# Kernel tuning notes

Measured on AMD Instinct MI355X. Metric: run time of the kernel, lower is better.

## Reference

```python
import jax, jax.numpy as jnp
import numpy as np

N_NODES = 100000
N_EDGES = 1600000
F_IN = 48
F_HID = 64


def setup_inputs() -> dict:
    key = jax.random.key(0)
    k1, k2, k3, k4 = jax.random.split(key, 4)
    x = jax.random.normal(k1, (N_NODES, F_IN), dtype=jnp.float32)
    edge_index = jax.random.randint(k2, (2, N_EDGES), 0, N_NODES, dtype=jnp.int64)
    W1 = jax.random.normal(k3, (F_IN, F_HID), dtype=jnp.float32) * (1.0 / np.sqrt(F_IN))
    b1 = jnp.zeros((F_HID,), dtype=jnp.float32)
    W2 = jax.random.normal(k4, (F_HID, 2), dtype=jnp.float32) * (1.0 / np.sqrt(F_HID))
    b2 = jnp.zeros((2,), dtype=jnp.float32)
    return {"x": x, "edge_index": edge_index, "W1": W1, "b1": b1, "W2": W2, "b2": b2}


def _gcn_prep(edge_index, n_nodes):
    # PyG GCNConv default: add self-loops, symmetric normalization D^-1/2 (A+I) D^-1/2
    loops = jnp.arange(n_nodes, dtype=edge_index.dtype)
    src = jnp.concatenate([edge_index[0], loops])
    dst = jnp.concatenate([edge_index[1], loops])
    deg = jax.ops.segment_sum(jnp.ones_like(dst, dtype=jnp.float32), dst,
                              num_segments=n_nodes)
    dinv = jnp.where(deg > 0, jax.lax.rsqrt(deg), 0.0)
    norm = dinv[src] * dinv[dst]  # [E+N]
    return src, dst, norm


def _gcn_conv(h, W, b, src, dst, norm, n_nodes):
    h = h @ W                          # [N, F_out] linear first (PyG order)
    msg = h[src] * norm[:, None]       # gather + edge-scale
    agg = jax.ops.segment_sum(msg, dst, num_segments=n_nodes)  # scatter-add
    return agg + b


def reference(x, edge_index, W1, b1, W2, b2):
    n = x.shape[0]
    src, dst, norm = _gcn_prep(edge_index, n)
    h = jax.nn.relu(_gcn_conv(x, W1, b1, src, dst, norm, n))
    return _gcn_conv(h, W2, b2, src, dst, norm, n)
```

## Files before the change

kernel.cpp:

```cpp
#include <hip/hip_runtime.h>
#include <hip/hip_fp16.h>

#define F_IN 48
#define F_HID 64
#define GSH 7
#define GSZ 128
#define MAXB 1024
#define CAPSH 12
#define CAP 4096
#define CHUNK 4096
#define NPW 16

__device__ __forceinline__ bool detect64(const int* __restrict__ e) {
    return ((e[1] | e[3] | e[5] | e[7]) == 0);
}
__device__ __forceinline__ int load_src(const int* e, int i, int E, bool is64) {
    return e[is64 ? (long)2 * i : (long)i];
}
__device__ __forceinline__ int load_dst(const int* e, int i, int E, bool is64) {
    return e[is64 ? (long)2 * (E + i) : (long)(E + i)];
}
__device__ __forceinline__ void fmix2(float& alo, float& ahi, unsigned h) {
    asm("v_fma_mix_f32 %0, %2, 1.0, %0 op_sel_hi:[1,0,0]\n\t"
        "v_fma_mix_f32 %1, %2, 1.0, %1 op_sel:[1,0,0] op_sel_hi:[1,0,0]"
        : "+v"(alo), "+v"(ahi) : "v"(h));
}

__global__ __launch_bounds__(256) void passA(const int* __restrict__ e,
                                             int* __restrict__ bcnt,
                                             int* __restrict__ ebuf, int E, int B) {
    __shared__ int lcnt[MAXB], lbase[MAXB];
    bool is64 = detect64(e);
    bool vec = ((E & 3) == 0);
    int base = blockIdx.x * CHUNK;
    for (int t = threadIdx.x; t < B; t += 256) lcnt[t] = 0;
    __syncthreads();
    int pk[16], bk[16], rk[16];
#pragma unroll
    for (int g = 0; g < 4; ++g) {
        int i = base + (((g << 8) + (int)threadIdx.x) << 2);
        int r = g * 4;
        if (vec && i + 3 < E) {
            int4 s4, d4;
            if (is64) {
                const int4* p = (const int4*)(e + (size_t)2 * i);
                int4 a = p[0], bb = p[1];
                s4 = make_int4(a.x, a.z, bb.x, bb.z);
                const int4* q = (const int4*)(e + (size_t)2 * E + (size_t)2 * i);
                int4 c = q[0], dd = q[1];
                d4 = make_int4(c.x, c.z, dd.x, dd.z);
            } else {
                s4 = *(const int4*)(e + i);
                d4 = *(const int4*)(e + E + i);
            }
            int ss[4] = {s4.x, s4.y, s4.z, s4.w};
            int dv[4] = {d4.x, d4.y, d4.z, d4.w};
#pragma unroll
            for (int u = 0; u < 4; ++u) {
                pk[r + u] = ss[u] | ((dv[u] & (GSZ - 1)) << 17);
                bk[r + u] = dv[u] >> GSH;
                rk[r + u] = atomicAdd(&lcnt[bk[r + u]], 1);
            }
        } else {
#pragma unroll
            for (int u = 0; u < 4; ++u) {
                int ii = i + u;
                if (ii < E) {
                    int s = load_src(e, ii, E, is64);
                    int d = load_dst(e, ii, E, is64);
                    pk[r + u] = s | ((d & (GSZ - 1)) << 17);
                    bk[r + u] = d >> GSH;
                    rk[r + u] = atomicAdd(&lcnt[bk[r + u]], 1);
                } else {
                    bk[r + u] = -1;
                }
            }
        }
    }
    __syncthreads();
    for (int t = threadIdx.x; t < B; t += 256) {
        int c = lcnt[t];
        lbase[t] = c ? atomicAdd(&bcnt[t], c) : 0;
    }
    __syncthreads();
#pragma unroll
    for (int r = 0; r < 16; ++r) {
        if (bk[r] >= 0) {
            int pos = lbase[bk[r]] + rk[r];
            if (pos < CAP) ebuf[((size_t)bk[r] << CAPSH) + pos] = pk[r];
        }
    }
}

__global__ __launch_bounds__(256) void passB(const int* __restrict__ ebuf,
                                             const int* __restrict__ bcnt,
                                             int* __restrict__ rowStart,
                                             int* __restrict__ deg,
                                             float* __restrict__ dinv,
                                             int* __restrict__ srcSorted, int N) {
    __shared__ int cnt[GSZ], inc[GSZ], exo[GSZ];
    int b = blockIdx.x, t = threadIdx.x;
    int m = min(bcnt[b], CAP);
    const int* eb = ebuf + ((size_t)b << CAPSH);
    if (t < GSZ) cnt[t] = 0;
    __syncthreads();
    int gk[16], sk[16], rk[16];
    int iters = (m + 255) >> 8;
    for (int it = 0; it < iters; ++it) {
        int i = t + (it << 8);
        if (i < m) {
            int pkv = eb[i];
            gk[it] = pkv >> 17;
            sk[it] = pkv & 0x1FFFF;
            rk[it] = atomicAdd(&cnt[gk[it]], 1);
        } else {
            gk[it] = -1;
        }
    }
    __syncthreads();
    int myc = (t < GSZ) ? cnt[t] : 0;
    if (t < GSZ) inc[t] = myc;
    __syncthreads();
    for (int o = 1; o < GSZ; o <<= 1) {
        int v = (t < GSZ && t >= o) ? inc[t - o] : 0;
        __syncthreads();
        if (t < GSZ) inc[t] += v;
        __syncthreads();
    }
    if (t < GSZ) {
        int ex = inc[t] - myc;
        exo[t] = ex;
        int node = (b << GSH) + t;
        if (node < N) {
            rowStart[node] = (b << CAPSH) + ex;
            deg[node] = myc;
            dinv[node] = rsqrtf((float)myc + 1.0f);
        }
    }
    __syncthreads();
    int s0b = b << CAPSH;
    for (int it = 0; it < iters; ++it) {
        if (gk[it] >= 0)
            srcSorted[s0b + exo[gk[it]] + rk[it]] = sk[it];
    }
}

__global__ __launch_bounds__(256) void gemm1(const float* __restrict__ x,
                                             const float* __restrict__ W1,
                                             const float* __restrict__ dinv,
                                             __half* __restrict__ H, int N) {
    const int lane = threadIdx.x & 63;
    const int warp = __builtin_amdgcn_readfirstlane((int)(threadIdx.x >> 6));
    const int nb = (blockIdx.x * 4 + warp) * NPW;
    float w[F_IN];
#pragma unroll
    for (int k = 0; k < F_IN; ++k) w[k] = W1[k * F_HID + lane];
    for (int u = 0; u < NPW; u += 2) {
        int na = nb + u, nb2 = nb + u + 1;
        int nac = min(na, N - 1), nbc = min(nb2, N - 1);
        const float* xra = x + (size_t)nac * F_IN;
        const float* xrb = x + (size_t)nbc * F_IN;
        float ha = 0.0f, hb = 0.0f;
#pragma unroll
        for (int k = 0; k < F_IN; ++k) {
            ha = fmaf(xra[k], w[k], ha);
            hb = fmaf(xrb[k], w[k], hb);
        }
        if (na < N)
            H[(size_t)na * F_HID + lane] = __float2half(dinv[nac] * ha);
        if (nb2 < N)
            H[(size_t)nb2 * F_HID + lane] = __float2half(dinv[nbc] * hb);
    }
}

__global__ __launch_bounds__(256) void agg1(const __half* __restrict__ H,
                                            const float* __restrict__ b1,
                                            const float* __restrict__ W2,
                                            const float* __restrict__ dinv,
                                            const int* __restrict__ rowStart,
                                            const int* __restrict__ deg,
                                            const int* __restrict__ srcSorted,
                                            float* __restrict__ g2, int N) {
    const int lane = threadIdx.x & 63;
    const int sub = lane >> 5;
    const int fl = lane & 31;
    const int base = blockIdx.x * 16 + (threadIdx.x >> 6) * 4;
    const char* hb = (const char*)H;
    const unsigned fb = (unsigned)fl << 2;

    int n0 = base, n1 = base + 1, n2 = base + 2, n3 = base + 3;
    int dn0 = (n0 < N) ? deg[n0] : -1;
    int dn1 = (n1 < N) ? deg[n1] : -1;
    int dn2_ = (n2 < N) ? deg[n2] : -1;
    int dn3 = (n3 < N) ? deg[n3] : -1;
    int rs0 = (n0 < N) ? rowStart[n0] : 0;
    int rs1 = (n1 < N) ? rowStart[n1] : 0;
    int rs2 = (n2 < N) ? rowStart[n2] : 0;
    int rs3 = (n3 < N) ? rowStart[n3] : 0;

    int idx0 = N, idx1 = N, idx2 = N, idx3 = N;
    if (lane < dn0) idx0 = srcSorted[rs0 + lane]; else if (lane == dn0) idx0 = n0;
    if (lane < dn1) idx1 = srcSorted[rs1 + lane]; else if (lane == dn1) idx1 = n1;
    if (lane < dn2_) idx2 = srcSorted[rs2 + lane]; else if (lane == dn2_) idx2 = n2;
    if (lane < dn3) idx3 = srcSorted[rs3 + lane]; else if (lane == dn3) idx3 = n3;

    float ax0 = 0, ay0 = 0, ax1 = 0, ay1 = 0;
    float ax2 = 0, ay2 = 0, ax3 = 0, ay3 = 0;

    auto batch6 = [&](int p0) {
        unsigned o[6][4], v[6][4];
#pragma unroll
        for (int p = 0; p < 6; ++p) {
            int sA = 2 * (p0 + p) + sub;
            o[p][0] = ((unsigned)__shfl(idx0, sA, 64) << 7) + fb;
            o[p][1] = ((unsigned)__shfl(idx1, sA, 64) << 7) + fb;
            o[p][2] = ((unsigned)__shfl(idx2, sA, 64) << 7) + fb;
            o[p][3] = ((unsigned)__shfl(idx3, sA, 64) << 7) + fb;
        }
#pragma unroll
        for (int p = 0; p < 6; ++p) {
            v[p][0] = *(const unsigned*)(hb + o[p][0]);
            v[p][1] = *(const unsigned*)(hb + o[p][1]);
            v[p][2] = *(const unsigned*)(hb + o[p][2]);
            v[p][3] = *(const unsigned*)(hb + o[p][3]);
        }
#pragma unroll
        for (int p = 0; p < 6; ++p) {
            fmix2(ax0, ay0, v[p][0]);
            fmix2(ax1, ay1, v[p][1]);
            fmix2(ax2, ay2, v[p][2]);
            fmix2(ax3, ay3, v[p][3]);
        }
    };
    batch6(0);
    batch6(6);

    int maxD = max(max(dn0, dn1), max(dn2_, dn3));
    int maxSlot = maxD + 1;
    for (int p = 12; p < 32 && 2 * p < maxSlot; ++p) {
        int sA = 2 * p + sub;
        unsigned o0 = ((unsigned)__shfl(idx0, sA, 64) << 7) + fb;
        unsigned o1 = ((unsigned)__shfl(idx1, sA, 64) << 7) + fb;
        unsigned o2 = ((unsigned)__shfl(idx2, sA, 64) << 7) + fb;
        unsigned o3 = ((unsigned)__shfl(idx3, sA, 64) << 7) + fb;
        unsigned v0 = *(const unsigned*)(hb + o0);
        unsigned v1 = *(const unsigned*)(hb + o1);
        unsigned v2 = *(const unsigned*)(hb + o2);
        unsigned v3 = *(const unsigned*)(hb + o3);
        fmix2(ax0, ay0, v0);
        fmix2(ax1, ay1, v1);
        fmix2(ax2, ay2, v2);
        fmix2(ax3, ay3, v3);
    }
    if (maxSlot > 64) {
        const __half2* hp = (const __half2*)H;
        for (int s = 64; s < maxSlot; ++s) {
            if (sub == 0) {
                if (s <= dn0) { float2 f = __half22float2(hp[((long)((s < dn0) ? srcSorted[rs0 + s] : n0) << 5) + fl]); ax0 += f.x; ay0 += f.y; }
                if (s <= dn1) { float2 f = __half22float2(hp[((long)((s < dn1) ? srcSorted[rs1 + s] : n1) << 5) + fl]); ax1 += f.x; ay1 += f.y; }
                if (s <= dn2_) { float2 f = __half22float2(hp[((long)((s < dn2_) ? srcSorted[rs2 + s] : n2) << 5) + fl]); ax2 += f.x; ay2 += f.y; }
                if (s <= dn3) { float2 f = __half22float2(hp[((long)((s < dn3) ? srcSorted[rs3 + s] : n3) << 5) + fl]); ax3 += f.x; ay3 += f.y; }
            }
        }
    }

    ax0 += __shfl(ax0, lane ^ 32, 64); ay0 += __shfl(ay0, lane ^ 32, 64);
    ax1 += __shfl(ax1, lane ^ 32, 64); ay1 += __shfl(ay1, lane ^ 32, 64);
    ax2 += __shfl(ax2, lane ^ 32, 64); ay2 += __shfl(ay2, lane ^ 32, 64);
    ax3 += __shfl(ax3, lane ^ 32, 64); ay3 += __shfl(ay3, lane ^ 32, 64);
    float di0 = (n0 < N) ? dinv[n0] : 0.0f;
    float di1 = (n1 < N) ? dinv[n1] : 0.0f;
    float di2 = (n2 < N) ? dinv[n2] : 0.0f;
    float di3 = (n3 < N) ? dinv[n3] : 0.0f;

    float2 b1v = *(const float2*)(b1 + 2 * fl);
    float4 w2q = *(const float4*)(W2 + 4 * fl);
    float hA, hB;
    hA = fmaxf(fmaf(di0, ax0, b1v.x), 0.0f); hB = fmaxf(fmaf(di0, ay0, b1v.y), 0.0f);
    float t00 = hA * w2q.x + hB * w2q.z, t01 = hA * w2q.y + hB * w2q.w;
    hA = fmaxf(fmaf(di1, ax1, b1v.x), 0.0f); hB = fmaxf(fmaf(di1, ay1, b1v.y), 0.0f);
    float t10 = hA * w2q.x + hB * w2q.z, t11 = hA * w2q.y + hB * w2q.w;
    hA = fmaxf(fmaf(di2, ax2, b1v.x), 0.0f); hB = fmaxf(fmaf(di2, ay2, b1v.y), 0.0f);
    float t20 = hA * w2q.x + hB * w2q.z, t21 = hA * w2q.y + hB * w2q.w;
    hA = fmaxf(fmaf(di3, ax3, b1v.x), 0.0f); hB = fmaxf(fmaf(di3, ay3, b1v.y), 0.0f);
    float t30 = hA * w2q.x + hB * w2q.z, t31 = hA * w2q.y + hB * w2q.w;
#pragma unroll
    for (int m = 1; m <= 16; m <<= 1) {
        t00 += __shfl_xor(t00, m, 64); t01 += __shfl_xor(t01, m, 64);
        t10 += __shfl_xor(t10, m, 64); t11 += __shfl_xor(t11, m, 64);
        t20 += __shfl_xor(t20, m, 64); t21 += __shfl_xor(t21, m, 64);
        t30 += __shfl_xor(t30, m, 64); t31 += __shfl_xor(t31, m, 64);
    }
    if (lane == 0) {
        float2* g2v = (float2*)g2;
        if (n0 < N) g2v[n0] = make_float2(di0 * t00, di0 * t01);
        if (n1 < N) g2v[n1] = make_float2(di1 * t10, di1 * t11);
        if (n2 < N) g2v[n2] = make_float2(di2 * t20, di2 * t21);
        if (n3 < N) g2v[n3] = make_float2(di3 * t30, di3 * t31);
    }
}

__global__ __launch_bounds__(256) void agg2(const int* __restrict__ rowStart,
                                            const int* __restrict__ deg,
                                            const int* __restrict__ srcSorted,
                                            const float* __restrict__ g2,
                                            const float* __restrict__ dinv,
                                            const float* __restrict__ b2,
                                            float* __restrict__ out, int N) {
    int gid = blockIdx.x * 256 + threadIdx.x;
    int node = gid >> 4, l16 = gid & 15;
    if (node >= N) return;
    const char* gb = (const char*)g2;
    int rs = rowStart[node], dn = deg[node];
    float a0 = 0.0f, a1 = 0.0f;
    for (int j = l16; j < dn; j += 16) {
        unsigned o = (unsigned)srcSorted[rs + j] << 3;
        float2 v = *(const float2*)(gb + o);
        a0 += v.x;
        a1 += v.y;
    }
#pragma unroll
    for (int m = 1; m < 16; m <<= 1) {
        a0 += __shfl_xor(a0, m, 64);
        a1 += __shfl_xor(a1, m, 64);
    }
    if (l16 == 0) {
        float2 self = *(const float2*)(gb + ((unsigned)node << 3));
        float di = dinv[node];
        out[2 * node + 0] = di * (a0 + self.x) + b2[0];
        out[2 * node + 1] = di * (a1 + self.y) + b2[1];
    }
}

extern "C" void kernel_launch(void* const* d_in, const int* in_sizes, int n_in,
                              void* d_out, int out_size, void* d_ws, size_t ws_size,
                              hipStream_t stream) {
    const float* x  = (const float*)d_in[0];
    const int* eidx = (const int*)d_in[1];
    const float* W1 = (const float*)d_in[2];
    const float* b1 = (const float*)d_in[3];
    const float* W2 = (const float*)d_in[4];
    const float* b2 = (const float*)d_in[5];
    float* out = (float*)d_out;

    int N = in_sizes[0] / F_IN;
    int E = in_sizes[1] / 2;
    int B = (N + GSZ - 1) >> GSH;

    char* ws = (char*)d_ws;
    __half* H         = (__half*)ws;   ws += (size_t)(N + 1) * F_HID * 2;
    int*    bcnt      = (int*)ws;      ws += MAXB * 4;
    int*    deg       = (int*)ws;      ws += (size_t)N * 4;
    int*    rowStart  = (int*)ws;      ws += (size_t)N * 4;
    float*  dinv      = (float*)ws;    ws += (size_t)N * 4;
    float*  g2        = (float*)ws;    ws += (size_t)N * 2 * 4;
    ws = (char*)(((size_t)ws + 255) & ~(size_t)255);
    int*    ebuf      = (int*)ws;      ws += (size_t)MAXB * CAP * 4;
    int*    srcSorted = (int*)ws;      ws += (size_t)MAXB * CAP * 4;

    hipMemsetAsync(H + (size_t)N * F_HID, 0, 128 + MAXB * 4, stream);

    passA<<<(E + CHUNK - 1) / CHUNK, 256, 0, stream>>>(eidx, bcnt, ebuf, E, B);
    passB<<<B, 256, 0, stream>>>(ebuf, bcnt, rowStart, deg, dinv, srcSorted, N);
    gemm1<<<(N + 4 * NPW - 1) / (4 * NPW), 256, 0, stream>>>(x, W1, dinv, H, N);
    agg1<<<(N + 15) / 16, 256, 0, stream>>>(H, b1, W2, dinv, rowStart, deg,
                                            srcSorted, g2, N);
    agg2<<<(N * 16 + 255) / 256, 256, 0, stream>>>(rowStart, deg, srcSorted, g2,
                                                   dinv, b2, out, N);
}
```

Before: 178.5 us.

## Fuse feature GEMM into CSR build pass and recompute dinv from degree

Folds the gemm1 kernel into passB so each 128-node bucket block also computes its nodes' H rows, reading dinv from shared memory instead of global. The dinv array is removed entirely and recomputed via rsqrt of the degree in agg1 and agg2. This saves one kernel launch and the dinv global write and reads. In exchange, passB blocks carry heavier register pressure from the 48 W1 weights, and the grid for the GEMM work shrinks to about 782 blocks.

```diff
diff --git a/kernel.cpp b/kernel.cpp
--- a/kernel.cpp
+++ b/kernel.cpp
@@ -9,7 +9,6 @@
 #define CAPSH 12
 #define CAP 4096
 #define CHUNK 4096
-#define NPW 16
 
 __device__ __forceinline__ bool detect64(const int* __restrict__ e) {
     return ((e[1] | e[3] | e[5] | e[7]) == 0);
@@ -92,13 +91,16 @@
     }
 }
 
-__global__ __launch_bounds__(256) void passB(const int* __restrict__ ebuf,
-                                             const int* __restrict__ bcnt,
-                                             int* __restrict__ rowStart,
-                                             int* __restrict__ deg,
-                                             float* __restrict__ dinv,
-                                             int* __restrict__ srcSorted, int N) {
+__global__ __launch_bounds__(256) void passBH(const int* __restrict__ ebuf,
+                                              const int* __restrict__ bcnt,
+                                              const float* __restrict__ x,
+                                              const float* __restrict__ W1,
+                                              int* __restrict__ rowStart,
+                                              int* __restrict__ deg,
+                                              int* __restrict__ srcSorted,
+                                              __half* __restrict__ H, int N) {
     __shared__ int cnt[GSZ], inc[GSZ], exo[GSZ];
+    __shared__ float ldinv[GSZ];
     int b = blockIdx.x, t = threadIdx.x;
     int m = min(bcnt[b], CAP);
     const int* eb = ebuf + ((size_t)b << CAPSH);
@@ -130,11 +132,11 @@
     if (t < GSZ) {
         int ex = inc[t] - myc;
         exo[t] = ex;
+        ldinv[t] = rsqrtf((float)myc + 1.0f);
         int node = (b << GSH) + t;
         if (node < N) {
             rowStart[node] = (b << CAPSH) + ex;
             deg[node] = myc;
-            dinv[node] = rsqrtf((float)myc + 1.0f);
         }
     }
     __syncthreads();
@@ -143,22 +145,18 @@
         if (gk[it] >= 0)
             srcSorted[s0b + exo[gk[it]] + rk[it]] = sk[it];
     }
-}
-
-__global__ __launch_bounds__(256) void gemm1(const float* __restrict__ x,
-                                             const float* __restrict__ W1,
-                                             const float* __restrict__ dinv,
-                                             __half* __restrict__ H, int N) {
-    const int lane = threadIdx.x & 63;
-    const int warp = __builtin_amdgcn_readfirstlane((int)(threadIdx.x >> 6));
-    const int nb = (blockIdx.x * 4 + warp) * NPW;
+    const int lane = t & 63;
+    const int warp = __builtin_amdgcn_readfirstlane(t >> 6);
     float w[F_IN];
 #pragma unroll
     for (int k = 0; k < F_IN; ++k) w[k] = W1[k * F_HID + lane];
-    for (int u = 0; u < NPW; u += 2) {
-        int na = nb + u, nb2 = nb + u + 1;
-        int nac = min(na, N - 1), nbc = min(nb2, N - 1);
-        const float* xra = x + (size_t)nac * F_IN;
+    const int lbase_n = warp << 5;
+    const int nodeBase = (b << GSH) + lbase_n;
+    for (int u = 0; u < 32; u += 2) {
+        int na = nodeBase + u, nb2 = nodeBase + u + 1;
+        if (na >= N) break;
+        int nbc = min(nb2, N - 1);
+        const float* xra = x + (size_t)na * F_IN;
         const float* xrb = x + (size_t)nbc * F_IN;
         float ha = 0.0f, hb = 0.0f;
 #pragma unroll
@@ -166,17 +164,16 @@
             ha = fmaf(xra[k], w[k], ha);
             hb = fmaf(xrb[k], w[k], hb);
         }
-        if (na < N)
-            H[(size_t)na * F_HID + lane] = __float2half(dinv[nac] * ha);
+        H[(size_t)na * F_HID + lane] = __float2half(ldinv[lbase_n + u] * ha);
         if (nb2 < N)
-            H[(size_t)nb2 * F_HID + lane] = __float2half(dinv[nbc] * hb);
+            H[(size_t)nb2 * F_HID + lane] =
+                __float2half(ldinv[lbase_n + u + 1] * hb);
     }
 }
 
 __global__ __launch_bounds__(256) void agg1(const __half* __restrict__ H,
                                             const float* __restrict__ b1,
                                             const float* __restrict__ W2,
-                                            const float* __restrict__ dinv,
                                             const int* __restrict__ rowStart,
                                             const int* __restrict__ deg,
                                             const int* __restrict__ srcSorted,
@@ -268,10 +265,10 @@
     ax1 += __shfl(ax1, lane ^ 32, 64); ay1 += __shfl(ay1, lane ^ 32, 64);
     ax2 += __shfl(ax2, lane ^ 32, 64); ay2 += __shfl(ay2, lane ^ 32, 64);
     ax3 += __shfl(ax3, lane ^ 32, 64); ay3 += __shfl(ay3, lane ^ 32, 64);
-    float di0 = (n0 < N) ? dinv[n0] : 0.0f;
-    float di1 = (n1 < N) ? dinv[n1] : 0.0f;
-    float di2 = (n2 < N) ? dinv[n2] : 0.0f;
-    float di3 = (n3 < N) ? dinv[n3] : 0.0f;
+    float di0 = (n0 < N) ? rsqrtf((float)dn0 + 1.0f) : 0.0f;
+    float di1 = (n1 < N) ? rsqrtf((float)dn1 + 1.0f) : 0.0f;
+    float di2 = (n2 < N) ? rsqrtf((float)dn2_ + 1.0f) : 0.0f;
+    float di3 = (n3 < N) ? rsqrtf((float)dn3 + 1.0f) : 0.0f;
 
     float2 b1v = *(const float2*)(b1 + 2 * fl);
     float4 w2q = *(const float4*)(W2 + 4 * fl);
@@ -304,7 +301,6 @@
                                             const int* __restrict__ deg,
                                             const int* __restrict__ srcSorted,
                                             const float* __restrict__ g2,
-                                            const float* __restrict__ dinv,
                                             const float* __restrict__ b2,
                                             float* __restrict__ out, int N) {
     int gid = blockIdx.x * 256 + threadIdx.x;
@@ -326,7 +322,7 @@
     }
     if (l16 == 0) {
         float2 self = *(const float2*)(gb + ((unsigned)node << 3));
-        float di = dinv[node];
+        float di = rsqrtf((float)dn + 1.0f);
         out[2 * node + 0] = di * (a0 + self.x) + b2[0];
         out[2 * node + 1] = di * (a1 + self.y) + b2[1];
     }
@@ -352,7 +348,6 @@
     int*    bcnt      = (int*)ws;      ws += MAXB * 4;
     int*    deg       = (int*)ws;      ws += (size_t)N * 4;
     int*    rowStart  = (int*)ws;      ws += (size_t)N * 4;
-    float*  dinv      = (float*)ws;    ws += (size_t)N * 4;
     float*  g2        = (float*)ws;    ws += (size_t)N * 2 * 4;
     ws = (char*)(((size_t)ws + 255) & ~(size_t)255);
     int*    ebuf      = (int*)ws;      ws += (size_t)MAXB * CAP * 4;
@@ -361,10 +356,10 @@
     hipMemsetAsync(H + (size_t)N * F_HID, 0, 128 + MAXB * 4, stream);
 
     passA<<<(E + CHUNK - 1) / CHUNK, 256, 0, stream>>>(eidx, bcnt, ebuf, E, B);
-    passB<<<B, 256, 0, stream>>>(ebuf, bcnt, rowStart, deg, dinv, srcSorted, N);
-    gemm1<<<(N + 4 * NPW - 1) / (4 * NPW), 256, 0, stream>>>(x, W1, dinv, H, N);
-    agg1<<<(N + 15) / 16, 256, 0, stream>>>(H, b1, W2, dinv, rowStart, deg,
-                                            srcSorted, g2, N);
+    passBH<<<B, 256, 0, stream>>>(ebuf, bcnt, x, W1, rowStart, deg, srcSorted,
+                                  H, N);
+    agg1<<<(N + 15) / 16, 256, 0, stream>>>(H, b1, W2, rowStart, deg, srcSorted,
+                                            g2, N);
     agg2<<<(N * 16 + 255) / 256, 256, 0, stream>>>(rowStart, deg, srcSorted, g2,
-                                                   dinv, b2, out, N);
-}
+                                                   b2, out, N);
+}
```

New measurement: 199.5 us. 1.12x slower.
